# Kernel optimization log

Hardware: AMD Instinct MI355X
Metric: run time of the kernel (lower is better)

Reference implementation:

```python
import math
import jax, jax.numpy as jnp
import numpy as np

TAR_MIN, TAR_MAX = 0.0, 1.0
SRC_MIN, SRC_MAX = 0.0, 1.0
NUM_BINS_TAR = 32
NUM_BINS_SRC = 32
SIGMA_TAR = 0.5 * (TAR_MAX - TAR_MIN) / NUM_BINS_TAR
SIGMA_SRC = 0.5 * (SRC_MAX - SRC_MIN) / NUM_BINS_SRC
EPS = 1e-10


def setup_inputs() -> dict:
    key = jax.random.key(0)
    k1, k2 = jax.random.split(key)
    shape = (4, 1, 96, 96, 96)
    tar = jax.random.uniform(k1, shape, dtype=jnp.float32)
    src = jax.random.uniform(k2, shape, dtype=jnp.float32)
    return {"tar": tar, "src": src}


def _minmax_normalise(x, min_out, max_out):
    # per-sample minmax over all non-batch dims; x: (N, P)
    mn = jnp.min(x, axis=1, keepdims=True)
    mx = jnp.max(x, axis=1, keepdims=True)
    return (x - mn) / (mx - mn + 1e-12) * (max_out - min_out) + min_out


def _window(x, bins, sigma):
    # x: (N, P); bins: (B,) -> (N, B, P) Gaussian soft-binning
    d = x[:, None, :] - bins[None, :, None]
    return jnp.exp(-(d * d) / (2.0 * sigma * sigma)) / math.sqrt(2.0 * math.pi) * sigma


def reference(tar, src):
    N = tar.shape[0]
    t = tar[:, 0].reshape(N, -1)  # (N, P)
    s = src[:, 0].reshape(N, -1)
    t = _minmax_normalise(t, TAR_MIN, TAR_MAX)
    s = _minmax_normalise(s, SRC_MIN, SRC_MAX)

    bins_tar = jnp.linspace(TAR_MIN, TAR_MAX, NUM_BINS_TAR, dtype=t.dtype)
    bins_src = jnp.linspace(SRC_MIN, SRC_MAX, NUM_BINS_SRC, dtype=s.dtype)

    wt = _window(t, bins_tar, SIGMA_TAR)  # (N, Bt, P)
    ws = _window(s, bins_src, SIGMA_SRC)  # (N, Bs, P)

    hist_joint = jnp.einsum('bip,bjp->bij', wt, ws)  # (N, Bt, Bs)
    hist_norm = jnp.sum(hist_joint, axis=(1, 2), keepdims=True)
    p_joint = hist_joint / hist_norm

    p_tar = jnp.sum(p_joint, axis=2)  # (N, Bt)
    p_src = jnp.sum(p_joint, axis=1)  # (N, Bs)

    ent_tar = -jnp.sum(p_tar * jnp.log(p_tar + EPS), axis=1)
    ent_src = -jnp.sum(p_src * jnp.log(p_src + EPS), axis=1)
    ent_joint = -jnp.sum(p_joint * jnp.log(p_joint + EPS), axis=(1, 2))

    # normalised=True
    return -jnp.mean((ent_tar + ent_src) / ent_joint)
```

## Files before the change

### kernel.cpp

```cpp
#include <hip/hip_runtime.h>
#include <hip/hip_cooperative_groups.h>
#include <math.h>

namespace cg = cooperative_groups;

#define N_SAMPLES 4
#define P_ELEMS   (96*96*96)
#define BPS       216
#define NBLOCKS   (N_SAMPLES * BPS)
#define TILE      4096
#define T4        (TILE/4)
#define WS        1.75343855f
#define EPSR      1e-10f

typedef __attribute__((ext_vector_type(8)))  short short8;
typedef __attribute__((ext_vector_type(16))) float float16;


__device__ __forceinline__ void load_chunk(const float* __restrict__ tar,
                                           const float* __restrict__ src,
                                           int n, int j, int t,
                                           float4 a[4], float4 b[4]) {
    const float4* t4 = (const float4*)(tar + (size_t)n * P_ELEMS) + (size_t)j * T4;
    const float4* s4 = (const float4*)(src + (size_t)n * P_ELEMS) + (size_t)j * T4;
    a[0] = t4[t]; a[1] = t4[t + 256]; a[2] = t4[t + 512]; a[3] = t4[t + 768];
    b[0] = s4[t]; b[1] = s4[t + 256]; b[2] = s4[t + 512]; b[3] = s4[t + 768];
}

__device__ __forceinline__ float4 block_minmax(const float4 a[4], const float4 b[4],
                                               int t, float4* sred) {
    float mnt = INFINITY, mxt = -INFINITY, mns = INFINITY, mxs = -INFINITY;
    #pragma unroll
    for (int r = 0; r < 4; r++) {
        mnt = fminf(mnt, fminf(fminf(a[r].x, a[r].y), fminf(a[r].z, a[r].w)));
        mxt = fmaxf(mxt, fmaxf(fmaxf(a[r].x, a[r].y), fmaxf(a[r].z, a[r].w)));
        mns = fminf(mns, fminf(fminf(b[r].x, b[r].y), fminf(b[r].z, b[r].w)));
        mxs = fmaxf(mxs, fmaxf(fmaxf(b[r].x, b[r].y), fmaxf(b[r].z, b[r].w)));
    }
    #pragma unroll
    for (int o = 32; o; o >>= 1) {
        mnt = fminf(mnt, __shfl_xor(mnt, o));
        mxt = fmaxf(mxt, __shfl_xor(mxt, o));
        mns = fminf(mns, __shfl_xor(mns, o));
        mxs = fmaxf(mxs, __shfl_xor(mxs, o));
    }
    int lane = t & 63, wave = t >> 6;
    if (lane == 0) sred[wave] = make_float4(mnt, mxt, mns, mxs);
    __syncthreads();
    float4 r = make_float4(0.f, 0.f, 0.f, 0.f);
    if (t == 0) {
        float4 v0 = sred[0], v1 = sred[1], v2 = sred[2], v3 = sred[3];
        r.x = fminf(fminf(v0.x, v1.x), fminf(v2.x, v3.x));
        r.y = fmaxf(fmaxf(v0.y, v1.y), fmaxf(v2.y, v3.y));
        r.z = fminf(fminf(v0.z, v1.z), fminf(v2.z, v3.z));
        r.w = fmaxf(fmaxf(v0.w, v1.w), fmaxf(v2.w, v3.w));
    }
    return r;
}

__device__ __forceinline__ float4 reduce_partials(const float4* __restrict__ pwn,
                                                  int t, float4* sred, float* bc) {
    float mnt = INFINITY, mxt = -INFINITY, mns = INFINITY, mxs = -INFINITY;
    if (t < BPS) {
        float4 v = pwn[t];
        mnt = v.x; mxt = v.y; mns = v.z; mxs = v.w;
    }
    #pragma unroll
    for (int o = 32; o; o >>= 1) {
        mnt = fminf(mnt, __shfl_xor(mnt, o));
        mxt = fmaxf(mxt, __shfl_xor(mxt, o));
        mns = fminf(mns, __shfl_xor(mns, o));
        mxs = fmaxf(mxs, __shfl_xor(mxs, o));
    }
    int lane = t & 63, wave = t >> 6;
    if (lane == 0) sred[wave] = make_float4(mnt, mxt, mns, mxs);
    __syncthreads();
    if (t == 0) {
        float4 v0 = sred[0], v1 = sred[1], v2 = sred[2], v3 = sred[3];
        bc[0] = fminf(fminf(v0.x, v1.x), fminf(v2.x, v3.x));
        bc[1] = fmaxf(fmaxf(v0.y, v1.y), fmaxf(v2.y, v3.y));
        bc[2] = fminf(fminf(v0.z, v1.z), fminf(v2.z, v3.z));
        bc[3] = fmaxf(fmaxf(v0.w, v1.w), fmaxf(v2.w, v3.w));
    }
    __syncthreads();
    return make_float4(bc[0], bc[1], bc[2], bc[3]);
}

__device__ __forceinline__ void hist_phase(float* lds,
                                           const float4 a[4], const float4 b[4],
                                           float mnt, float fit, float mns, float fis,
                                           float* __restrict__ histn, int t) {
    #pragma unroll
    for (int r = 0; r < 4; r++) {
        float4 xo, yo;
        xo.x = (a[r].x - mnt) * fit; xo.y = (a[r].y - mnt) * fit;
        xo.z = (a[r].z - mnt) * fit; xo.w = (a[r].w - mnt) * fit;
        yo.x = (b[r].x - mns) * fis; yo.y = (b[r].y - mns) * fis;
        yo.z = (b[r].z - mns) * fis; yo.w = (b[r].w - mns) * fis;
        ((float4*)lds)[t + r * 256] = xo;
        ((float4*)(lds + TILE))[t + r * 256] = yo;
    }
    __syncthreads();

    int lane = t & 63, wave = t >> 6, g = lane >> 5;
    float q = (float)(lane & 31) * WS;
    const float* xb = lds + wave * 1024;
    const float* yb = lds + TILE + wave * 1024;

    float16 acc;
    #pragma unroll
    for (int i = 0; i < 16; i++) acc[i] = 0.0f;

    #pragma unroll 2
    for (int it = 0; it < 64; it++) {
        int kb = it * 16 + g * 8;
        float4 xa = *(const float4*)(xb + kb);
        float4 xc = *(const float4*)(xb + kb + 4);
        float4 ya = *(const float4*)(yb + kb);
        float4 yc = *(const float4*)(yb + kb + 4);
        float xs[8] = {xa.x, xa.y, xa.z, xa.w, xc.x, xc.y, xc.z, xc.w};
        float ys[8] = {ya.x, ya.y, ya.z, ya.w, yc.x, yc.y, yc.z, yc.w};
        unsigned av[8], bv[8];
        #pragma unroll
        for (int jj = 0; jj < 8; jj++) {
            float d = xs[jj] - q;
            float arg = -d * d;
            float w;
            asm("v_exp_f32 %0, %1" : "=v"(w) : "v"(arg));
            av[jj] = __float_as_uint(w);
            d = ys[jj] - q;
            arg = -d * d;
            asm("v_exp_f32 %0, %1" : "=v"(w) : "v"(arg));
            bv[jj] = __float_as_uint(w);
        }
        union { unsigned u[4]; short8 v; } af, bf;
        #pragma unroll
        for (int jj = 0; jj < 4; jj++) {
            af.u[jj] = __builtin_amdgcn_perm(av[2 * jj + 1], av[2 * jj], 0x07060302u);
            bf.u[jj] = __builtin_amdgcn_perm(bv[2 * jj + 1], bv[2 * jj], 0x07060302u);
        }
        acc = __builtin_amdgcn_mfma_f32_32x32x16_bf16(af.v, bf.v, acc, 0, 0, 0);
    }

    __syncthreads();
    {
        float* hw = lds + wave * 1024;
        int col = lane & 31;
        #pragma unroll
        for (int reg = 0; reg < 16; reg++) {
            int row = (reg & 3) + 8 * (reg >> 2) + 4 * g;
            hw[row * 32 + col] = acc[reg];
        }
    }
    __syncthreads();
    for (int bb = t; bb < 1024; bb += 256) {
        float v = lds[bb] + lds[1024 + bb] + lds[2048 + bb] + lds[3072 + bb];
        unsafeAtomicAdd(&histn[bb], v);
    }
}

__device__ __forceinline__ void finalize_phase(const float* __restrict__ hist,
                                               float* sh, float* __restrict__ out, int t) {
    __shared__ float wres[4];
    int lane = t & 63, nn = t >> 6;
    const float4* h4 = (const float4*)(hist + nn * 1024);
    float4 h[4];
    float part = 0.0f;
    #pragma unroll
    for (int r = 0; r < 4; r++) {
        h[r] = h4[lane * 4 + r];
        part += (h[r].x + h[r].y) + (h[r].z + h[r].w);
    }
    #pragma unroll
    for (int o = 32; o; o >>= 1) part += __shfl_xor(part, o);
    float inv = 1.0f / part;
    float ej = 0.0f;
    #pragma unroll
    for (int r = 0; r < 4; r++) {
        float4 p;
        p.x = h[r].x * inv; p.y = h[r].y * inv; p.z = h[r].z * inv; p.w = h[r].w * inv;
        ((float4*)(sh + nn * 1024))[lane * 4 + r] = p;
        ej -= p.x * __logf(p.x + EPSR) + p.y * __logf(p.y + EPSR)
            + p.z * __logf(p.z + EPSR) + p.w * __logf(p.w + EPSR);
    }
    #pragma unroll
    for (int o = 32; o; o >>= 1) ej += __shfl_xor(ej, o);
    __syncthreads();
    float m = 0.0f;
    if (lane < 32) {
        int row = lane;
        for (int jj = 0; jj < 32; jj++) m += sh[nn * 1024 + row * 32 + ((jj + row) & 31)];
    } else {
        int col = lane - 32;
        for (int i = 0; i < 32; i++) m += sh[nn * 1024 + i * 32 + col];
    }
    float rc = -m * __logf(m + EPSR);
    #pragma unroll
    for (int o = 16; o; o >>= 1) rc += __shfl_xor(rc, o);
    float es = __shfl(rc, 32);
    if (lane == 0) wres[nn] = (rc + es) / ej;
    __syncthreads();
    if (t == 0)
        out[0] = -(wres[0] + wres[1] + wres[2] + wres[3]) * 0.25f;
}


__global__ void __launch_bounds__(256, 4)
mi_fused(const float* __restrict__ tar, const float* __restrict__ src,
         float4* __restrict__ pw, float* __restrict__ hist,
         float* __restrict__ out) {
    cg::grid_group grid = cg::this_grid();
    __shared__ __align__(16) float lds[2 * TILE];
    __shared__ float4 sred[4];
    __shared__ float bc[4];

    int bid = blockIdx.x;
    int n = bid / BPS, j = bid - n * BPS;
    int t = threadIdx.x;

    float4 a[4], b[4];
    load_chunk(tar, src, n, j, t, a, b);
    float4 mm = block_minmax(a, b, t, sred);
    if (t == 0) pw[bid] = mm;
    if (bid < 16) hist[bid * 256 + t] = 0.0f;
    grid.sync();

    float4 M = reduce_partials(pw + n * BPS, t, sred, bc);
    float fit = 31.0f * WS / (M.y - M.x + 1e-12f);
    float fis = 31.0f * WS / (M.w - M.z + 1e-12f);
    hist_phase(lds, a, b, M.x, fit, M.z, fis, hist + n * 1024, t);
    grid.sync();

    if (bid == 0) finalize_phase(hist, lds, out, t);
}


__global__ void __launch_bounds__(256, 4)
k_minmax(const float* __restrict__ tar, const float* __restrict__ src,
         float4* __restrict__ pw, float* __restrict__ hist) {
    __shared__ float4 sred[4];
    int n = blockIdx.y, j = blockIdx.x, bid = n * BPS + j;
    int t = threadIdx.x;
    float4 a[4], b[4];
    load_chunk(tar, src, n, j, t, a, b);
    float4 mm = block_minmax(a, b, t, sred);
    if (t == 0) pw[bid] = mm;
    if (bid < 16) hist[bid * 256 + t] = 0.0f;
}

__global__ void __launch_bounds__(256, 4)
k_hist(const float* __restrict__ tar, const float* __restrict__ src,
       const float4* __restrict__ pw, float* __restrict__ hist) {
    __shared__ __align__(16) float lds[2 * TILE];
    __shared__ float4 sred[4];
    __shared__ float bc[4];
    int n = blockIdx.y, j = blockIdx.x;
    int t = threadIdx.x;
    float4 M = reduce_partials(pw + n * BPS, t, sred, bc);
    float fit = 31.0f * WS / (M.y - M.x + 1e-12f);
    float fis = 31.0f * WS / (M.w - M.z + 1e-12f);
    float4 a[4], b[4];
    load_chunk(tar, src, n, j, t, a, b);
    hist_phase(lds, a, b, M.x, fit, M.z, fis, hist + n * 1024, t);
}

__global__ void __launch_bounds__(256)
k_final(const float* __restrict__ hist, float* __restrict__ out) {
    __shared__ float sh[4096];
    finalize_phase(hist, sh, out, threadIdx.x);
}

extern "C" void kernel_launch(void* const* d_in, const int* in_sizes, int n_in,
                              void* d_out, int out_size, void* d_ws, size_t ws_size,
                              hipStream_t stream) {
    const float* tar = (const float*)d_in[0];
    const float* src = (const float*)d_in[1];
    float* out = (float*)d_out;
    float4* pw = (float4*)d_ws;
    float* hist = (float*)((char*)d_ws + NBLOCKS * 16);

    int occ = 0, ncu = 0, dev = 0;
    hipError_t qe = hipOccupancyMaxActiveBlocksPerMultiprocessor(&occ, mi_fused, 256, 0);
    hipGetDevice(&dev);
    hipDeviceGetAttribute(&ncu, hipDeviceAttributeMultiprocessorCount, dev);
    bool coop_ok = (qe == hipSuccess) && (ncu > 0) && ((long)occ * ncu >= NBLOCKS);

    if (coop_ok) {
        void* args[] = { (void*)&tar, (void*)&src, (void*)&pw, (void*)&hist, (void*)&out };
        hipError_t e = hipLaunchCooperativeKernel((void*)mi_fused, dim3(NBLOCKS), dim3(256),
                                                  args, 0, stream);
        if (e == hipSuccess) return;
    }
    k_minmax<<<dim3(BPS, N_SAMPLES), 256, 0, stream>>>(tar, src, pw, hist);
    k_hist<<<dim3(BPS, N_SAMPLES), 256, 0, stream>>>(tar, src, pw, hist);
    k_final<<<1, 256, 0, stream>>>(hist, out);
}
```

Before: 112.1 us.

## Replace cooperative fused kernel with three launches, smaller hist tiles, replicated histograms

```diff
diff --git a/kernel.cpp b/kernel.cpp
--- a/kernel.cpp
+++ b/kernel.cpp
@@ -1,42 +1,49 @@
 #include <hip/hip_runtime.h>
-#include <hip/hip_cooperative_groups.h>
 #include <math.h>
-
-namespace cg = cooperative_groups;
 
 #define N_SAMPLES 4
 #define P_ELEMS   (96*96*96)
-#define BPS       216
-#define NBLOCKS   (N_SAMPLES * BPS)
-#define TILE      4096
-#define T4        (TILE/4)
+#define MM_BPS    216
+#define MM_T4     1024
+#define H_BPS     432
+#define H_TILE    2048
+#define H_T4      (H_TILE/4)
+#define NCOPY     8
 #define WS        1.75343855f
 #define EPSR      1e-10f
 
 typedef __attribute__((ext_vector_type(8)))  short short8;
 typedef __attribute__((ext_vector_type(16))) float float16;
 
-
-__device__ __forceinline__ void load_chunk(const float* __restrict__ tar,
-                                           const float* __restrict__ src,
-                                           int n, int j, int t,
-                                           float4 a[4], float4 b[4]) {
-    const float4* t4 = (const float4*)(tar + (size_t)n * P_ELEMS) + (size_t)j * T4;
-    const float4* s4 = (const float4*)(src + (size_t)n * P_ELEMS) + (size_t)j * T4;
-    a[0] = t4[t]; a[1] = t4[t + 256]; a[2] = t4[t + 512]; a[3] = t4[t + 768];
-    b[0] = s4[t]; b[1] = s4[t + 256]; b[2] = s4[t + 512]; b[3] = s4[t + 768];
-}
-
-__device__ __forceinline__ float4 block_minmax(const float4 a[4], const float4 b[4],
-                                               int t, float4* sred) {
-    float mnt = INFINITY, mxt = -INFINITY, mns = INFINITY, mxs = -INFINITY;
-    #pragma unroll
-    for (int r = 0; r < 4; r++) {
-        mnt = fminf(mnt, fminf(fminf(a[r].x, a[r].y), fminf(a[r].z, a[r].w)));
-        mxt = fmaxf(mxt, fmaxf(fmaxf(a[r].x, a[r].y), fmaxf(a[r].z, a[r].w)));
-        mns = fminf(mns, fminf(fminf(b[r].x, b[r].y), fminf(b[r].z, b[r].w)));
-        mxs = fmaxf(mxs, fmaxf(fmaxf(b[r].x, b[r].y), fmaxf(b[r].z, b[r].w)));
-    }
+#define PW_COUNT  (N_SAMPLES * H_BPS)
+
+
+__global__ void __launch_bounds__(256)
+k_minmax(const float* __restrict__ tar, const float* __restrict__ src,
+         float4* __restrict__ pw, float* __restrict__ histall) {
+    __shared__ float4 sred[4];
+    int n = blockIdx.y, j = blockIdx.x;
+    int t = threadIdx.x;
+    const float4* t4 = (const float4*)(tar + (size_t)n * P_ELEMS) + (size_t)j * MM_T4;
+    const float4* s4 = (const float4*)(src + (size_t)n * P_ELEMS) + (size_t)j * MM_T4;
+    float4 a0 = t4[t], a1 = t4[t + 256], a2 = t4[t + 512], a3 = t4[t + 768];
+    float4 b0 = s4[t], b1 = s4[t + 256], b2 = s4[t + 512], b3 = s4[t + 768];
+    float mnt = fminf(fminf(fminf(a0.x, a0.y), fminf(a0.z, a0.w)),
+                      fminf(fminf(a1.x, a1.y), fminf(a1.z, a1.w)));
+    mnt = fminf(mnt, fminf(fminf(fminf(a2.x, a2.y), fminf(a2.z, a2.w)),
+                           fminf(fminf(a3.x, a3.y), fminf(a3.z, a3.w))));
+    float mxt = fmaxf(fmaxf(fmaxf(a0.x, a0.y), fmaxf(a0.z, a0.w)),
+                      fmaxf(fmaxf(a1.x, a1.y), fmaxf(a1.z, a1.w)));
+    mxt = fmaxf(mxt, fmaxf(fmaxf(fmaxf(a2.x, a2.y), fmaxf(a2.z, a2.w)),
+                           fmaxf(fmaxf(a3.x, a3.y), fmaxf(a3.z, a3.w))));
+    float mns = fminf(fminf(fminf(b0.x, b0.y), fminf(b0.z, b0.w)),
+                      fminf(fminf(b1.x, b1.y), fminf(b1.z, b1.w)));
+    mns = fminf(mns, fminf(fminf(fminf(b2.x, b2.y), fminf(b2.z, b2.w)),
+                           fminf(fminf(b3.x, b3.y), fminf(b3.z, b3.w))));
+    float mxs = fmaxf(fmaxf(fmaxf(b0.x, b0.y), fmaxf(b0.z, b0.w)),
+                      fmaxf(fmaxf(b1.x, b1.y), fmaxf(b1.z, b1.w)));
+    mxs = fmaxf(mxs, fmaxf(fmaxf(fmaxf(b2.x, b2.y), fmaxf(b2.z, b2.w)),
+                           fmaxf(fmaxf(b3.x, b3.y), fmaxf(b3.z, b3.w))));
     #pragma unroll
     for (int o = 32; o; o >>= 1) {
         mnt = fminf(mnt, __shfl_xor(mnt, o));
@@ -47,72 +54,92 @@
     int lane = t & 63, wave = t >> 6;
     if (lane == 0) sred[wave] = make_float4(mnt, mxt, mns, mxs);
     __syncthreads();
-    float4 r = make_float4(0.f, 0.f, 0.f, 0.f);
     if (t == 0) {
         float4 v0 = sred[0], v1 = sred[1], v2 = sred[2], v3 = sred[3];
+        float4 r;
         r.x = fminf(fminf(v0.x, v1.x), fminf(v2.x, v3.x));
         r.y = fmaxf(fmaxf(v0.y, v1.y), fmaxf(v2.y, v3.y));
         r.z = fminf(fminf(v0.z, v1.z), fminf(v2.z, v3.z));
         r.w = fmaxf(fmaxf(v0.w, v1.w), fmaxf(v2.w, v3.w));
-    }
-    return r;
-}
-
-__device__ __forceinline__ float4 reduce_partials(const float4* __restrict__ pwn,
-                                                  int t, float4* sred, float* bc) {
-    float mnt = INFINITY, mxt = -INFINITY, mns = INFINITY, mxs = -INFINITY;
-    if (t < BPS) {
-        float4 v = pwn[t];
-        mnt = v.x; mxt = v.y; mns = v.z; mxs = v.w;
-    }
-    #pragma unroll
-    for (int o = 32; o; o >>= 1) {
-        mnt = fminf(mnt, __shfl_xor(mnt, o));
-        mxt = fmaxf(mxt, __shfl_xor(mxt, o));
-        mns = fminf(mns, __shfl_xor(mns, o));
-        mxs = fmaxf(mxs, __shfl_xor(mxs, o));
-    }
-    int lane = t & 63, wave = t >> 6;
-    if (lane == 0) sred[wave] = make_float4(mnt, mxt, mns, mxs);
-    __syncthreads();
-    if (t == 0) {
-        float4 v0 = sred[0], v1 = sred[1], v2 = sred[2], v3 = sred[3];
-        bc[0] = fminf(fminf(v0.x, v1.x), fminf(v2.x, v3.x));
-        bc[1] = fmaxf(fmaxf(v0.y, v1.y), fmaxf(v2.y, v3.y));
-        bc[2] = fminf(fminf(v0.z, v1.z), fminf(v2.z, v3.z));
-        bc[3] = fmaxf(fmaxf(v0.w, v1.w), fmaxf(v2.w, v3.w));
-    }
-    __syncthreads();
-    return make_float4(bc[0], bc[1], bc[2], bc[3]);
-}
-
-__device__ __forceinline__ void hist_phase(float* lds,
-                                           const float4 a[4], const float4 b[4],
-                                           float mnt, float fit, float mns, float fis,
-                                           float* __restrict__ histn, int t) {
-    #pragma unroll
-    for (int r = 0; r < 4; r++) {
+        pw[n * MM_BPS + j] = r;
+    }
+    int bid = n * MM_BPS + j;
+    if (bid < 128) histall[bid * 256 + t] = 0.0f;
+}
+
+
+__global__ void __launch_bounds__(256, 8)
+k_hist(const float* __restrict__ tar, const float* __restrict__ src,
+       const float4* __restrict__ pw, float* __restrict__ histall) {
+    __shared__ __align__(16) float lds[2 * H_TILE];
+    __shared__ float4 sred[4];
+    __shared__ float bc[4];
+    int n = blockIdx.y, j = blockIdx.x;
+    int t = threadIdx.x;
+
+    const float4* t4 = (const float4*)(tar + (size_t)n * P_ELEMS) + (size_t)j * H_T4;
+    const float4* s4 = (const float4*)(src + (size_t)n * P_ELEMS) + (size_t)j * H_T4;
+    float4 a0 = t4[t], a1 = t4[t + 256];
+    float4 b0 = s4[t], b1 = s4[t + 256];
+
+    {
+        const float4* pwn = pw + n * MM_BPS;
+        float mnt = INFINITY, mxt = -INFINITY, mns = INFINITY, mxs = -INFINITY;
+        if (t < MM_BPS) {
+            float4 v = pwn[t];
+            mnt = v.x; mxt = v.y; mns = v.z; mxs = v.w;
+        }
+        #pragma unroll
+        for (int o = 32; o; o >>= 1) {
+            mnt = fminf(mnt, __shfl_xor(mnt, o));
+            mxt = fmaxf(mxt, __shfl_xor(mxt, o));
+            mns = fminf(mns, __shfl_xor(mns, o));
+            mxs = fmaxf(mxs, __shfl_xor(mxs, o));
+        }
+        int lane = t & 63, wave = t >> 6;
+        if (lane == 0) sred[wave] = make_float4(mnt, mxt, mns, mxs);
+        __syncthreads();
+        if (t == 0) {
+            float4 v0 = sred[0], v1 = sred[1], v2 = sred[2], v3 = sred[3];
+            bc[0] = fminf(fminf(v0.x, v1.x), fminf(v2.x, v3.x));
+            bc[1] = fmaxf(fmaxf(v0.y, v1.y), fmaxf(v2.y, v3.y));
+            bc[2] = fminf(fminf(v0.z, v1.z), fminf(v2.z, v3.z));
+            bc[3] = fmaxf(fmaxf(v0.w, v1.w), fmaxf(v2.w, v3.w));
+        }
+        __syncthreads();
+    }
+    float mnt = bc[0], mns = bc[2];
+    float fit = 31.0f * WS / (bc[1] - mnt + 1e-12f);
+    float fis = 31.0f * WS / (bc[3] - mns + 1e-12f);
+
+    {
         float4 xo, yo;
-        xo.x = (a[r].x - mnt) * fit; xo.y = (a[r].y - mnt) * fit;
-        xo.z = (a[r].z - mnt) * fit; xo.w = (a[r].w - mnt) * fit;
-        yo.x = (b[r].x - mns) * fis; yo.y = (b[r].y - mns) * fis;
-        yo.z = (b[r].z - mns) * fis; yo.w = (b[r].w - mns) * fis;
-        ((float4*)lds)[t + r * 256] = xo;
-        ((float4*)(lds + TILE))[t + r * 256] = yo;
+        xo.x = (a0.x - mnt) * fit; xo.y = (a0.y - mnt) * fit;
+        xo.z = (a0.z - mnt) * fit; xo.w = (a0.w - mnt) * fit;
+        ((float4*)lds)[t] = xo;
+        xo.x = (a1.x - mnt) * fit; xo.y = (a1.y - mnt) * fit;
+        xo.z = (a1.z - mnt) * fit; xo.w = (a1.w - mnt) * fit;
+        ((float4*)lds)[t + 256] = xo;
+        yo.x = (b0.x - mns) * fis; yo.y = (b0.y - mns) * fis;
+        yo.z = (b0.z - mns) * fis; yo.w = (b0.w - mns) * fis;
+        ((float4*)(lds + H_TILE))[t] = yo;
+        yo.x = (b1.x - mns) * fis; yo.y = (b1.y - mns) * fis;
+        yo.z = (b1.z - mns) * fis; yo.w = (b1.w - mns) * fis;
+        ((float4*)(lds + H_TILE))[t + 256] = yo;
     }
     __syncthreads();
 
     int lane = t & 63, wave = t >> 6, g = lane >> 5;
     float q = (float)(lane & 31) * WS;
-    const float* xb = lds + wave * 1024;
-    const float* yb = lds + TILE + wave * 1024;
+    const float* xb = lds + wave * (H_TILE / 4);
+    const float* yb = lds + H_TILE + wave * (H_TILE / 4);
 
     float16 acc;
     #pragma unroll
     for (int i = 0; i < 16; i++) acc[i] = 0.0f;
 
-    #pragma unroll 2
-    for (int it = 0; it < 64; it++) {
+    #pragma unroll 4
+    for (int it = 0; it < H_TILE / 4 / 16; it++) {
         int kb = it * 16 + g * 8;
         float4 xa = *(const float4*)(xb + kb);
         float4 xc = *(const float4*)(xb + kb + 4);
@@ -153,23 +180,33 @@
         }
     }
     __syncthreads();
+    float* histn = histall + ((j & (NCOPY - 1)) * N_SAMPLES + n) * 1024;
     for (int bb = t; bb < 1024; bb += 256) {
         float v = lds[bb] + lds[1024 + bb] + lds[2048 + bb] + lds[3072 + bb];
         unsafeAtomicAdd(&histn[bb], v);
     }
 }
 
-__device__ __forceinline__ void finalize_phase(const float* __restrict__ hist,
-                                               float* sh, float* __restrict__ out, int t) {
+
+__global__ void __launch_bounds__(256)
+k_final(const float* __restrict__ histall, float* __restrict__ out) {
+    __shared__ float sh[4096];
     __shared__ float wres[4];
+    int t = threadIdx.x;
     int lane = t & 63, nn = t >> 6;
-    const float4* h4 = (const float4*)(hist + nn * 1024);
     float4 h[4];
     float part = 0.0f;
     #pragma unroll
     for (int r = 0; r < 4; r++) {
-        h[r] = h4[lane * 4 + r];
-        part += (h[r].x + h[r].y) + (h[r].z + h[r].w);
+        float4 s = make_float4(0.f, 0.f, 0.f, 0.f);
+        #pragma unroll
+        for (int c = 0; c < NCOPY; c++) {
+            const float4* h4 = (const float4*)(histall + (c * N_SAMPLES + nn) * 1024);
+            float4 v = h4[lane * 4 + r];
+            s.x += v.x; s.y += v.y; s.z += v.z; s.w += v.w;
+        }
+        h[r] = s;
+        part += (s.x + s.y) + (s.z + s.w);
     }
     #pragma unroll
     for (int o = 32; o; o >>= 1) part += __shfl_xor(part, o);
@@ -204,72 +241,6 @@
         out[0] = -(wres[0] + wres[1] + wres[2] + wres[3]) * 0.25f;
 }
 
-
-__global__ void __launch_bounds__(256, 4)
-mi_fused(const float* __restrict__ tar, const float* __restrict__ src,
-         float4* __restrict__ pw, float* __restrict__ hist,
-         float* __restrict__ out) {
-    cg::grid_group grid = cg::this_grid();
-    __shared__ __align__(16) float lds[2 * TILE];
-    __shared__ float4 sred[4];
-    __shared__ float bc[4];
-
-    int bid = blockIdx.x;
-    int n = bid / BPS, j = bid - n * BPS;
-    int t = threadIdx.x;
-
-    float4 a[4], b[4];
-    load_chunk(tar, src, n, j, t, a, b);
-    float4 mm = block_minmax(a, b, t, sred);
-    if (t == 0) pw[bid] = mm;
-    if (bid < 16) hist[bid * 256 + t] = 0.0f;
-    grid.sync();
-
-    float4 M = reduce_partials(pw + n * BPS, t, sred, bc);
-    float fit = 31.0f * WS / (M.y - M.x + 1e-12f);
-    float fis = 31.0f * WS / (M.w - M.z + 1e-12f);
-    hist_phase(lds, a, b, M.x, fit, M.z, fis, hist + n * 1024, t);
-    grid.sync();
-
-    if (bid == 0) finalize_phase(hist, lds, out, t);
-}
-
-
-__global__ void __launch_bounds__(256, 4)
-k_minmax(const float* __restrict__ tar, const float* __restrict__ src,
-         float4* __restrict__ pw, float* __restrict__ hist) {
-    __shared__ float4 sred[4];
-    int n = blockIdx.y, j = blockIdx.x, bid = n * BPS + j;
-    int t = threadIdx.x;
-    float4 a[4], b[4];
-    load_chunk(tar, src, n, j, t, a, b);
-    float4 mm = block_minmax(a, b, t, sred);
-    if (t == 0) pw[bid] = mm;
-    if (bid < 16) hist[bid * 256 + t] = 0.0f;
-}
-
-__global__ void __launch_bounds__(256, 4)
-k_hist(const float* __restrict__ tar, const float* __restrict__ src,
-       const float4* __restrict__ pw, float* __restrict__ hist) {
-    __shared__ __align__(16) float lds[2 * TILE];
-    __shared__ float4 sred[4];
-    __shared__ float bc[4];
-    int n = blockIdx.y, j = blockIdx.x;
-    int t = threadIdx.x;
-    float4 M = reduce_partials(pw + n * BPS, t, sred, bc);
-    float fit = 31.0f * WS / (M.y - M.x + 1e-12f);
-    float fis = 31.0f * WS / (M.w - M.z + 1e-12f);
-    float4 a[4], b[4];
-    load_chunk(tar, src, n, j, t, a, b);
-    hist_phase(lds, a, b, M.x, fit, M.z, fis, hist + n * 1024, t);
-}
-
-__global__ void __launch_bounds__(256)
-k_final(const float* __restrict__ hist, float* __restrict__ out) {
-    __shared__ float sh[4096];
-    finalize_phase(hist, sh, out, threadIdx.x);
-}
-
 extern "C" void kernel_launch(void* const* d_in, const int* in_sizes, int n_in,
                               void* d_out, int out_size, void* d_ws, size_t ws_size,
                               hipStream_t stream) {
@@ -277,21 +248,9 @@
     const float* src = (const float*)d_in[1];
     float* out = (float*)d_out;
     float4* pw = (float4*)d_ws;
-    float* hist = (float*)((char*)d_ws + NBLOCKS * 16);
-
-    int occ = 0, ncu = 0, dev = 0;
-    hipError_t qe = hipOccupancyMaxActiveBlocksPerMultiprocessor(&occ, mi_fused, 256, 0);
-    hipGetDevice(&dev);
-    hipDeviceGetAttribute(&ncu, hipDeviceAttributeMultiprocessorCount, dev);
-    bool coop_ok = (qe == hipSuccess) && (ncu > 0) && ((long)occ * ncu >= NBLOCKS);
-
-    if (coop_ok) {
-        void* args[] = { (void*)&tar, (void*)&src, (void*)&pw, (void*)&hist, (void*)&out };
-        hipError_t e = hipLaunchCooperativeKernel((void*)mi_fused, dim3(NBLOCKS), dim3(256),
-                                                  args, 0, stream);
-        if (e == hipSuccess) return;
-    }
-    k_minmax<<<dim3(BPS, N_SAMPLES), 256, 0, stream>>>(tar, src, pw, hist);
-    k_hist<<<dim3(BPS, N_SAMPLES), 256, 0, stream>>>(tar, src, pw, hist);
-    k_final<<<1, 256, 0, stream>>>(hist, out);
-}
+    float* histall = (float*)((char*)d_ws + PW_COUNT * 16);
+
+    k_minmax<<<dim3(MM_BPS, N_SAMPLES), 256, 0, stream>>>(tar, src, pw, histall);
+    k_hist<<<dim3(H_BPS, N_SAMPLES), 256, 0, stream>>>(tar, src, pw, histall);
+    k_final<<<1, 256, 0, stream>>>(histall, out);
+}
```

Measured after the change: 111.6 us. About the same (-0.4%).
